# Kernel tuning notes

Hardware: AMD Instinct MI355X
Metric: run time of the kernel (lower is better)

## Reference

```python
import jax, jax.numpy as jnp
import numpy as np
import math

B, L, E, H = 512, 200, 64, 4
D = E // H
NEG = jnp.float32(-(2.0 ** 32) + 1.0)


def setup_inputs() -> dict:
    key = jax.random.key(0)
    ks = jax.random.split(key, 12)
    inp = jax.random.normal(ks[0], (B, L, E), dtype=jnp.float32)
    # realistic variable-length histories: mask[b, t] = t < len_b, len_b in [1, L]
    lens = jax.random.randint(ks[1], (B, 1), 1, L + 1)
    mask = jnp.arange(L)[None, :] < lens  # [B, L] bool
    s = 1.0 / math.sqrt(E)
    pos_enc = jax.random.normal(ks[2], (1, L, E), dtype=jnp.float32)
    Wk = jax.random.uniform(ks[3], (E, E), jnp.float32, -s, s)
    bk = jnp.zeros((E,), jnp.float32)
    Wv = jax.random.uniform(ks[4], (E, E), jnp.float32, -s, s)
    bv = jnp.zeros((E,), jnp.float32)
    Wq = jax.random.uniform(ks[5], (E, E), jnp.float32, -s, s)
    bq = jnp.zeros((E,), jnp.float32)
    Wf = jax.random.uniform(ks[6], (E, E), jnp.float32, -s, s)
    bf = jnp.zeros((E,), jnp.float32)
    return {"input": inp, "mask": mask, "pos_enc": pos_enc,
            "Wk": Wk, "bk": bk, "Wv": Wv, "bv": bv,
            "Wq": Wq, "bq": bq, "Wf": Wf, "bf": bf}


def reference(input, mask, pos_enc, Wk, bk, Wv, bv, Wq, bq, Wf, bf):
    x = input + pos_enc  # [B, L, E]
    # project and split heads: [B, H, L, D]
    def split(t):
        return t.reshape(B, L, H, D).transpose(0, 2, 1, 3)
    k = split(x @ Wk.T + bk)
    v = split(x @ Wv.T + bv)
    q = split(x @ Wq.T + bq) / math.sqrt(D)
    scores = jnp.einsum('bhqd,bhkd->bhqk', q, k)  # [B, H, L, L]
    # key_mask in torch code broadcasts over dim 3 (mask on the QUERY axis),
    # query_mask is its transpose (mask on the KEY axis). Combined: both must be valid.
    both = mask[:, None, :, None] & mask[:, None, None, :]  # [B, 1, L, L]
    scores = jnp.where(both, scores, NEG)
    attn = jax.nn.softmax(scores, axis=-1)
    # dropout is identity at inference; omitted deterministically
    out = jnp.einsum('bhqk,bhkd->bhqd', attn, v)
    out = out.transpose(0, 2, 1, 3).reshape(B, L, E)
    out = out @ Wf.T + bf
    fm = mask.astype(jnp.float32)[:, :, None]  # [B, L, 1]
    lens = jnp.sum(fm, axis=1)  # [B, 1]
    pooled = jnp.sum(out * fm, axis=1) / (lens + 1e-8)  # [B, E]
    return pooled
```

## Files before the change

kernel.cpp:

```cpp
#include <hip/hip_runtime.h>
#include <hip/hip_fp16.h>
#include <math.h>

#define Bn 512
#define Ln 200
#define En 64
#define Hn 4
#define Dn 16
#define KS3 18
#define VS3 200
#define QSC 0.36067376022224085f

typedef _Float16 __f16;
typedef __fp16 fp16x2 __attribute__((ext_vector_type(2)));
typedef __f16 f16x4 __attribute__((ext_vector_type(4)));
typedef __f16 f16x8 __attribute__((ext_vector_type(8)));
typedef float f32x4 __attribute__((ext_vector_type(4)));

#if __has_builtin(__builtin_amdgcn_exp2f)
__device__ __forceinline__ float fexp2(float x) { return __builtin_amdgcn_exp2f(x); }
#else
__device__ __forceinline__ float fexp2(float x) { return exp2f(x); }
#endif

__device__ __forceinline__ f16x8 pack8s(float4 a, float4 b, float4 pa, float4 pb) {
    f16x8 r;
    r[0] = (__f16)(a.x + pa.x); r[1] = (__f16)(a.y + pa.y);
    r[2] = (__f16)(a.z + pa.z); r[3] = (__f16)(a.w + pa.w);
    r[4] = (__f16)(b.x + pb.x); r[5] = (__f16)(b.y + pb.y);
    r[6] = (__f16)(b.z + pb.z); r[7] = (__f16)(b.w + pb.w);
    return r;
}
__device__ __forceinline__ f16x8 pack8(float4 a, float4 b) {
    f16x8 r;
    r[0] = (__f16)a.x; r[1] = (__f16)a.y; r[2] = (__f16)a.z; r[3] = (__f16)a.w;
    r[4] = (__f16)b.x; r[5] = (__f16)b.y; r[6] = (__f16)b.z; r[7] = (__f16)b.w;
    return r;
}

__device__ __forceinline__ f16x4 pack4rtz(float e0, float e1, float e2, float e3) {
    const fp16x2 lo = __builtin_amdgcn_cvt_pkrtz(e0, e1);
    const fp16x2 hi = __builtin_amdgcn_cvt_pkrtz(e2, e3);
    f16x4 r;
    r[0] = (__f16)lo[0]; r[1] = (__f16)lo[1];
    r[2] = (__f16)hi[0]; r[3] = (__f16)hi[1];
    return r;
}

template<int NI>
__device__ __forceinline__ void attn_core(
    const __f16* __restrict__ Kh_, const __f16* __restrict__ Qh_, const __f16* __restrict__ Vt_,
    int qt0, int klo, int khi, int nt, int len, int quad, int ln16,
    f32x4 (&o2)[4], f32x4 (&lacc)[4])
{
    const f16x4 ones = {(__f16)1.f, (__f16)1.f, (__f16)1.f, (__f16)1.f};
    f16x4 qf[NI];
    #pragma unroll
    for (int i = 0; i < NI; ++i) {
        int qr = min((qt0 + i) * 16 + ln16, Ln - 1);
        qf[i] = *(const f16x4*)(Qh_ + qr * KS3 + quad * 4);
    }
    const bool needmask = (khi == nt);
    const int kfull = khi - (needmask ? 1 : 0);

    f16x4 kf = *(const f16x4*)(Kh_ + min(klo * 16 + ln16, Ln - 1) * KS3 + quad * 4);
    f16x4 vf = *(const f16x4*)(Vt_ + ln16 * VS3 + min(klo * 16 + quad * 4, Ln - 4));

    for (int kt = klo; kt < kfull; ++kt) {
        const int krn = min((kt + 1) * 16 + ln16, Ln - 1);
        const int vcn = min((kt + 1) * 16 + quad * 4, Ln - 4);
        const f16x4 kfn = *(const f16x4*)(Kh_ + krn * KS3 + quad * 4);
        const f16x4 vfn = *(const f16x4*)(Vt_ + ln16 * VS3 + vcn);
        f32x4 s[NI];
        #pragma unroll
        for (int i = 0; i < NI; ++i)
            s[i] = __builtin_amdgcn_mfma_f32_16x16x16f16(kf, qf[i], (f32x4){0,0,0,0}, 0, 0, 0);
        f16x4 pf[NI];
        #pragma unroll
        for (int i = 0; i < NI; ++i) {
            pf[i] = pack4rtz(fexp2(fminf(s[i][0], 14.5f)),
                             fexp2(fminf(s[i][1], 14.5f)),
                             fexp2(fminf(s[i][2], 14.5f)),
                             fexp2(fminf(s[i][3], 14.5f)));
        }
        #pragma unroll
        for (int i = 0; i < NI; ++i) {
            o2[i]   = __builtin_amdgcn_mfma_f32_16x16x16f16(vf,   pf[i], o2[i],   0, 0, 0);
            lacc[i] = __builtin_amdgcn_mfma_f32_16x16x16f16(ones, pf[i], lacc[i], 0, 0, 0);
        }
        kf = kfn; vf = vfn;
    }
    if (needmask) {
        const int kbase = (nt - 1) * 16 + quad * 4;
        f32x4 s[NI];
        #pragma unroll
        for (int i = 0; i < NI; ++i)
            s[i] = __builtin_amdgcn_mfma_f32_16x16x16f16(kf, qf[i], (f32x4){0,0,0,0}, 0, 0, 0);
        f16x4 pf[NI];
        #pragma unroll
        for (int i = 0; i < NI; ++i) {
            float e[4];
            #pragma unroll
            for (int j = 0; j < 4; ++j) {
                const bool kok = (kbase + j) < len;
                e[j] = kok ? fexp2(fminf(s[i][j], 14.5f)) : 0.f;
            }
            pf[i] = pack4rtz(e[0], e[1], e[2], e[3]);
        }
        #pragma unroll
        for (int i = 0; i < NI; ++i) {
            o2[i]   = __builtin_amdgcn_mfma_f32_16x16x16f16(vf,   pf[i], o2[i],   0, 0, 0);
            lacc[i] = __builtin_amdgcn_mfma_f32_16x16x16f16(ones, pf[i], lacc[i], 0, 0, 0);
        }
    }
}

__global__ __launch_bounds__(256, 4) void fused_kernel(
    const float* __restrict__ input, const int* __restrict__ mask,
    const float* __restrict__ pos_enc,
    const float* __restrict__ Wk, const float* __restrict__ bk,
    const float* __restrict__ Wv, const float* __restrict__ bv,
    const float* __restrict__ Wq, const float* __restrict__ bq,
    const float* __restrict__ Wf, const float* __restrict__ bf_,
    float* __restrict__ out)
{
    __shared__ __align__(16) __f16 Kh[Ln * KS3];
    __shared__ __align__(16) __f16 Qh[Ln * KS3];
    __shared__ __align__(16) __f16 Vt[16 * VS3];
    __shared__ float lred[4][4][16];
    __shared__ float red[4][16];
    __shared__ float ph[16];
    __shared__ int cnt_red[4];

    const int tid  = threadIdx.x;
    const int qh   = blockIdx.x & 1;
    const int bh   = blockIdx.x >> 1;
    const int b    = bh >> 2, h = bh & 3;
    const int wave = tid >> 6, lane = tid & 63;
    const int quad = lane >> 4, ln16 = lane & 15;

    const int mv = (tid < Ln) ? mask[b * Ln + tid] : 0;

    int c = (mv != 0) ? 1 : 0;
    #pragma unroll
    for (int off = 32; off; off >>= 1) c += __shfl_down(c, off, 64);
    if (lane == 0) cnt_red[wave] = c;
    __syncthreads();
    const int len = cnt_red[0] + cnt_red[1] + cnt_red[2] + cnt_red[3];
    const int nt = (len + 15) >> 4;
    const int nquad = (nt + 3) >> 2;
    const bool split = (nquad >= 3);

    if (qh == 1 && !split) return;

    f16x8 bfr[3][2];
    #pragma unroll
    for (int m = 0; m < 3; ++m) {
        const float* W = (m == 0) ? Wk : (m == 1) ? Wv : Wq;
        #pragma unroll
        for (int ks = 0; ks < 2; ++ks) {
            const float4* wp = (const float4*)(W + (size_t)(h * 16 + ln16) * 64) + (ks * 8 + quad * 2);
            bfr[m][ks] = pack8(wp[0], wp[1]);
        }
    }
    const int cg = h * 16 + ln16;
    const float bkv = bk[cg], bvv = bv[cg], bqv = bq[cg];

    const float4* in4 = (const float4*)(input + (size_t)b * Ln * En);
    const float4* pe4 = (const float4*)pos_enc;

    for (int rt = wave; rt < nt; rt += 4) {
        const int R = rt * 16 + ln16;
        const bool rok = (R < Ln);
        f16x8 af[2];
        #pragma unroll
        for (int ks = 0; ks < 2; ++ks) {
            float4 xa = {0,0,0,0}, xb = {0,0,0,0}, pa = {0,0,0,0}, pb = {0,0,0,0};
            if (rok) {
                const int o4 = R * 16 + ks * 8 + quad * 2;
                xa = in4[o4]; xb = in4[o4 + 1];
                pa = pe4[o4]; pb = pe4[o4 + 1];
            }
            af[ks] = pack8s(xa, xb, pa, pb);
        }
        f32x4 acc[3];
        #pragma unroll
        for (int m = 0; m < 3; ++m) acc[m] = (f32x4){0,0,0,0};
        #pragma unroll
        for (int ks = 0; ks < 2; ++ks)
            #pragma unroll
            for (int m = 0; m < 3; ++m)
                acc[m] = __builtin_amdgcn_mfma_f32_16x16x32_f16(af[ks], bfr[m][ks], acc[m], 0, 0, 0);

        #pragma unroll
        for (int j = 0; j < 4; ++j) {
            const int t = rt * 16 + quad * 4 + j;
            if (t < Ln) {
                Kh[t * KS3 + ln16] = (__f16)(acc[0][j] + bkv);
                Qh[t * KS3 + ln16] = (__f16)((acc[2][j] + bqv) * QSC);
            }
        }
        const int vc0 = rt * 16 + quad * 4;
        if (vc0 < Ln) {
            f16x4 vp;
            #pragma unroll
            for (int j = 0; j < 4; ++j) vp[j] = (__f16)(acc[1][j] + bvv);
            *(f16x4*)(Vt + ln16 * VS3 + vc0) = vp;
        }
    }
    __syncthreads();

    int g, kh, nkh;
    if (split)            { g = qh + 2 * (wave & 1); kh = wave >> 1; nkh = 2; }
    else if (nquad == 2)  { g = wave & 1;            kh = wave >> 1; nkh = 2; }
    else                  { g = 0;                   kh = wave;      nkh = 4; }
    const bool active = (g < nquad);
    const int nktp = (nt + nkh - 1) / nkh;
    const int klo = kh * nktp;
    const int khi = min(klo + nktp, nt);
    const int qt0 = 4 * g;

    f32x4 o2[4], lacc[4];
    #pragma unroll
    for (int i = 0; i < 4; ++i) { o2[i] = (f32x4){0,0,0,0}; lacc[i] = (f32x4){0,0,0,0}; }

    if (active && klo < khi) {
        const int ni = __builtin_amdgcn_readfirstlane(min(4, nt - qt0));
        switch (ni) {
            case 1:  attn_core<1>(Kh, Qh, Vt, qt0, klo, khi, nt, len, quad, ln16, o2, lacc); break;
            case 2:  attn_core<2>(Kh, Qh, Vt, qt0, klo, khi, nt, len, quad, ln16, o2, lacc); break;
            case 3:  attn_core<3>(Kh, Qh, Vt, qt0, klo, khi, nt, len, quad, ln16, o2, lacc); break;
            default: attn_core<4>(Kh, Qh, Vt, qt0, klo, khi, nt, len, quad, ln16, o2, lacc); break;
        }
    }

    float l[4];
    #pragma unroll
    for (int i = 0; i < 4; ++i) l[i] = lacc[i][0];

    if (nkh > 1) {
        if (lane < 16) {
            #pragma unroll
            for (int i = 0; i < 4; ++i) lred[wave][i][lane] = l[i];
        }
        __syncthreads();
        const int slot = wave & 1;
        #pragma unroll
        for (int i = 0; i < 4; ++i) {
            if (nkh == 2) l[i] = lred[slot][i][ln16] + lred[slot + 2][i][ln16];
            else          l[i] = lred[0][i][ln16] + lred[1][i][ln16]
                               + lred[2][i][ln16] + lred[3][i][ln16];
        }
    }

    f32x4 pool = {0.f, 0.f, 0.f, 0.f};
    if (active) {
        #pragma unroll
        for (int i = 0; i < 4; ++i) {
            const float rs = ((qt0 + i) * 16 + ln16 < len) ? 1.f / l[i] : 0.f;
            #pragma unroll
            for (int j = 0; j < 4; ++j) pool[j] = fmaf(o2[i][j], rs, pool[j]);
        }
    }

    #pragma unroll
    for (int j = 0; j < 4; ++j) {
        #pragma unroll
        for (int off = 1; off < 16; off <<= 1) pool[j] += __shfl_xor(pool[j], off, 64);
    }
    if (ln16 == 0) {
        #pragma unroll
        for (int j = 0; j < 4; ++j) red[wave][quad * 4 + j] = pool[j];
    }
    __syncthreads();
    if (tid < 16)
        ph[tid] = (red[0][tid] + red[1][tid] + red[2][tid] + red[3][tid]) / ((float)len + 1e-8f);
    __syncthreads();

    if (tid < 64) {
        const int e = tid;
        const float* wr = Wf + (size_t)e * 64 + h * 16;
        float a = (h == 0 && qh == 0) ? bf_[e] : 0.f;
        #pragma unroll
        for (int i = 0; i < 16; ++i) a = fmaf(wr[i], ph[i], a);
        atomicAdd(out + b * En + e, a);
    }
}

extern "C" void kernel_launch(void* const* d_in, const int* in_sizes, int n_in,
                              void* d_out, int out_size, void* d_ws, size_t ws_size,
                              hipStream_t stream) {
    const float* input   = (const float*)d_in[0];
    const int*   mask    = (const int*)  d_in[1];
    const float* pos_enc = (const float*)d_in[2];
    const float* Wk      = (const float*)d_in[3];
    const float* bk      = (const float*)d_in[4];
    const float* Wv      = (const float*)d_in[5];
    const float* bv      = (const float*)d_in[6];
    const float* Wq      = (const float*)d_in[7];
    const float* bq      = (const float*)d_in[8];
    const float* Wf      = (const float*)d_in[9];
    const float* bf      = (const float*)d_in[10];

    float* out = (float*)d_out;
    hipMemsetAsync(out, 0, (size_t)Bn * En * sizeof(float), stream);

    fused_kernel<<<Bn * Hn * 2, 256, 0, stream>>>(input, mask, pos_enc,
                                                  Wk, bk, Wv, bv, Wq, bq, Wf, bf, out);
}
```

Before: 144.5 us.

## Use persistent producer/consumer crews with double-buffered QKV projection and attention

Replaces the one-block-per-(batch,head,half) launch with a persistent grid of 768 blocks of 512 threads. One 256-thread crew computes the QKV projection for the next item into a double-buffered LDS slot while the other crew runs attention and pooling on the current item. Each wave now owns a query group and covers all key tiles, which removes the cross-wave softmax-denominator reduction and the query-half split. The aim is to overlap global loads and projection with attention and to cut launch and per-block overhead. In exchange, LDS use doubles, the static item split can leave load imbalance across blocks, and each wave issues its own atomics.

Result: no change. 144.1 us (-0.3%).

```diff
diff --git a/kernel.cpp b/kernel.cpp
--- a/kernel.cpp
+++ b/kernel.cpp
@@ -6,7 +6,8 @@
 #define Ln 200
 #define En 64
 #define Hn 4
-#define Dn 16
+#define NITEMS (Bn * Hn)
+#define GRID 768
 #define KS3 18
 #define VS3 200
 #define QSC 0.36067376022224085f
@@ -115,7 +116,7 @@
     }
 }
 
-__global__ __launch_bounds__(256, 4) void fused_kernel(
+__global__ __launch_bounds__(512, 6) void fused_kernel(
     const float* __restrict__ input, const int* __restrict__ mask,
     const float* __restrict__ pos_enc,
     const float* __restrict__ Wk, const float* __restrict__ bk,
@@ -124,166 +125,159 @@
     const float* __restrict__ Wf, const float* __restrict__ bf_,
     float* __restrict__ out)
 {
-    __shared__ __align__(16) __f16 Kh[Ln * KS3];
-    __shared__ __align__(16) __f16 Qh[Ln * KS3];
-    __shared__ __align__(16) __f16 Vt[16 * VS3];
-    __shared__ float lred[4][4][16];
-    __shared__ float red[4][16];
-    __shared__ float ph[16];
-    __shared__ int cnt_red[4];
+    __shared__ __align__(16) __f16 KhB[2][Ln * KS3];
+    __shared__ __align__(16) __f16 QhB[2][Ln * KS3];
+    __shared__ __align__(16) __f16 VtB[2][16 * VS3];
+    __shared__ float swr[4][16];
+    __shared__ int meta[2];
 
     const int tid  = threadIdx.x;
-    const int qh   = blockIdx.x & 1;
-    const int bh   = blockIdx.x >> 1;
-    const int b    = bh >> 2, h = bh & 3;
-    const int wave = tid >> 6, lane = tid & 63;
+    const int crew = tid >> 8;
+    const int wv   = (tid >> 6) & 3;
+    const int lane = tid & 63;
     const int quad = lane >> 4, ln16 = lane & 15;
 
-    const int mv = (tid < Ln) ? mask[b * Ln + tid] : 0;
-
-    int c = (mv != 0) ? 1 : 0;
-    #pragma unroll
-    for (int off = 32; off; off >>= 1) c += __shfl_down(c, off, 64);
-    if (lane == 0) cnt_red[wave] = c;
-    __syncthreads();
-    const int len = cnt_red[0] + cnt_red[1] + cnt_red[2] + cnt_red[3];
-    const int nt = (len + 15) >> 4;
-    const int nquad = (nt + 3) >> 2;
-    const bool split = (nquad >= 3);
-
-    if (qh == 1 && !split) return;
-
-    f16x8 bfr[3][2];
-    #pragma unroll
-    for (int m = 0; m < 3; ++m) {
-        const float* W = (m == 0) ? Wk : (m == 1) ? Wv : Wq;
-        #pragma unroll
-        for (int ks = 0; ks < 2; ++ks) {
-            const float4* wp = (const float4*)(W + (size_t)(h * 16 + ln16) * 64) + (ks * 8 + quad * 2);
-            bfr[m][ks] = pack8(wp[0], wp[1]);
-        }
-    }
-    const int cg = h * 16 + ln16;
-    const float bkv = bk[cg], bvv = bv[cg], bqv = bq[cg];
-
-    const float4* in4 = (const float4*)(input + (size_t)b * Ln * En);
+    const int lin = (blockIdx.x & 7) * (GRID / 8) + (blockIdx.x >> 3);
+    const int m   = (lin < NITEMS - 2 * GRID) ? 3 : 2;
+
     const float4* pe4 = (const float4*)pos_enc;
 
-    for (int rt = wave; rt < nt; rt += 4) {
-        const int R = rt * 16 + ln16;
-        const bool rok = (R < Ln);
-        f16x8 af[2];
-        #pragma unroll
-        for (int ks = 0; ks < 2; ++ks) {
-            float4 xa = {0,0,0,0}, xb = {0,0,0,0}, pa = {0,0,0,0}, pb = {0,0,0,0};
-            if (rok) {
-                const int o4 = R * 16 + ks * 8 + quad * 2;
-                xa = in4[o4]; xb = in4[o4 + 1];
-                pa = pe4[o4]; pb = pe4[o4 + 1];
+    for (int j = -1; j < m; ++j) {
+        if (crew == 0) {
+            const int r = j + 1;
+            if (r < m) {
+                const int item = lin + r * GRID;
+                const int b = item >> 2, h = item & 3;
+                __f16* Kh = KhB[r & 1];
+                __f16* Qh = QhB[r & 1];
+                __f16* Vt = VtB[r & 1];
+                const float4* in4 = (const float4*)(input + (size_t)b * Ln * En);
+
+                const int* mb = mask + b * Ln;
+                int c = (mb[lane] != 0) + (mb[64 + lane] != 0) + (mb[128 + lane] != 0)
+                      + ((lane < Ln - 192) ? (mb[192 + lane] != 0) : 0);
+                #pragma unroll
+                for (int off = 32; off; off >>= 1) c += __shfl_down(c, off, 64);
+                const int len = __shfl(c, 0, 64);
+                const int nt = (len + 15) >> 4;
+                if (tid == 0) meta[r & 1] = len;
+
+                f16x8 bfr[3][2];
+                #pragma unroll
+                for (int mm = 0; mm < 3; ++mm) {
+                    const float* W = (mm == 0) ? Wk : (mm == 1) ? Wv : Wq;
+                    #pragma unroll
+                    for (int ks = 0; ks < 2; ++ks) {
+                        const float4* wp = (const float4*)(W + (size_t)(h * 16 + ln16) * 64) + (ks * 8 + quad * 2);
+                        bfr[mm][ks] = pack8(wp[0], wp[1]);
+                    }
+                }
+                const int cg = h * 16 + ln16;
+                const float bkv = bk[cg], bvv = bv[cg], bqv = bq[cg];
+
+                for (int rt = wv; rt < nt; rt += 4) {
+                    const int R = rt * 16 + ln16;
+                    const bool rok = (R < Ln);
+                    const int o4 = R * 16 + quad * 2;
+                    float4 xa = {0,0,0,0}, xb = {0,0,0,0}, xc = {0,0,0,0}, xd = {0,0,0,0};
+                    float4 pa = {0,0,0,0}, pb = {0,0,0,0}, pc = {0,0,0,0}, pd = {0,0,0,0};
+                    if (rok) {
+                        xa = in4[o4];     xb = in4[o4 + 1];
+                        xc = in4[o4 + 8]; xd = in4[o4 + 9];
+                        pa = pe4[o4];     pb = pe4[o4 + 1];
+                        pc = pe4[o4 + 8]; pd = pe4[o4 + 9];
+                    }
+                    const f16x8 af0 = pack8s(xa, xb, pa, pb);
+                    const f16x8 af1 = pack8s(xc, xd, pc, pd);
+
+                    f32x4 acc[3];
+                    #pragma unroll
+                    for (int mm = 0; mm < 3; ++mm) acc[mm] = (f32x4){0,0,0,0};
+                    #pragma unroll
+                    for (int mm = 0; mm < 3; ++mm)
+                        acc[mm] = __builtin_amdgcn_mfma_f32_16x16x32_f16(af0, bfr[mm][0], acc[mm], 0, 0, 0);
+                    #pragma unroll
+                    for (int mm = 0; mm < 3; ++mm)
+                        acc[mm] = __builtin_amdgcn_mfma_f32_16x16x32_f16(af1, bfr[mm][1], acc[mm], 0, 0, 0);
+
+                    #pragma unroll
+                    for (int jj = 0; jj < 4; ++jj) {
+                        const int t = rt * 16 + quad * 4 + jj;
+                        if (t < Ln) {
+                            Kh[t * KS3 + ln16] = (__f16)(acc[0][jj] + bkv);
+                            Qh[t * KS3 + ln16] = (__f16)((acc[2][jj] + bqv) * QSC);
+                        }
+                    }
+                    const int vc0 = rt * 16 + quad * 4;
+                    if (vc0 < Ln) {
+                        f16x4 vp;
+                        #pragma unroll
+                        for (int jj = 0; jj < 4; ++jj) vp[jj] = (__f16)(acc[1][jj] + bvv);
+                        *(f16x4*)(Vt + ln16 * VS3 + vc0) = vp;
+                    }
+                }
             }
-            af[ks] = pack8s(xa, xb, pa, pb);
-        }
-        f32x4 acc[3];
-        #pragma unroll
-        for (int m = 0; m < 3; ++m) acc[m] = (f32x4){0,0,0,0};
-        #pragma unroll
-        for (int ks = 0; ks < 2; ++ks)
-            #pragma unroll
-            for (int m = 0; m < 3; ++m)
-                acc[m] = __builtin_amdgcn_mfma_f32_16x16x32_f16(af[ks], bfr[m][ks], acc[m], 0, 0, 0);
-
-        #pragma unroll
-        for (int j = 0; j < 4; ++j) {
-            const int t = rt * 16 + quad * 4 + j;
-            if (t < Ln) {
-                Kh[t * KS3 + ln16] = (__f16)(acc[0][j] + bkv);
-                Qh[t * KS3 + ln16] = (__f16)((acc[2][j] + bqv) * QSC);
+        } else {
+            if (j >= 0) {
+                const int item = lin + j * GRID;
+                const int b = item >> 2, h = item & 3;
+                const __f16* Kh = KhB[j & 1];
+                const __f16* Qh = QhB[j & 1];
+                const __f16* Vt = VtB[j & 1];
+                const int len = meta[j & 1];
+                const int nt = (len + 15) >> 4;
+                const int nquad = (nt + 3) >> 2;
+                const int g = wv;
+                const int qt0 = 4 * g;
+                const bool active = (g < nquad);
+
+                f32x4 o2[4], lacc[4];
+                #pragma unroll
+                for (int i = 0; i < 4; ++i) { o2[i] = (f32x4){0,0,0,0}; lacc[i] = (f32x4){0,0,0,0}; }
+
+                if (active) {
+                    const int ni = __builtin_amdgcn_readfirstlane(min(4, nt - qt0));
+                    switch (ni) {
+                        case 1:  attn_core<1>(Kh, Qh, Vt, qt0, 0, nt, nt, len, quad, ln16, o2, lacc); break;
+                        case 2:  attn_core<2>(Kh, Qh, Vt, qt0, 0, nt, nt, len, quad, ln16, o2, lacc); break;
+                        case 3:  attn_core<3>(Kh, Qh, Vt, qt0, 0, nt, nt, len, quad, ln16, o2, lacc); break;
+                        default: attn_core<4>(Kh, Qh, Vt, qt0, 0, nt, nt, len, quad, ln16, o2, lacc); break;
+                    }
+                }
+
+                f32x4 pool = {0.f, 0.f, 0.f, 0.f};
+                if (active) {
+                    #pragma unroll
+                    for (int i = 0; i < 4; ++i) {
+                        const float rs = ((qt0 + i) * 16 + ln16 < len) ? 1.f / lacc[i][0] : 0.f;
+                        #pragma unroll
+                        for (int jj = 0; jj < 4; ++jj) pool[jj] = fmaf(o2[i][jj], rs, pool[jj]);
+                    }
+                }
+                #pragma unroll
+                for (int jj = 0; jj < 4; ++jj) {
+                    #pragma unroll
+                    for (int off = 1; off < 16; off <<= 1) pool[jj] += __shfl_xor(pool[jj], off, 64);
+                }
+                if (ln16 == 0) {
+                    #pragma unroll
+                    for (int jj = 0; jj < 4; ++jj) swr[wv][quad * 4 + jj] = pool[jj];
+                }
+                float phv[16];
+                #pragma unroll
+                for (int i = 0; i < 16; ++i) phv[i] = swr[wv][i];
+
+                const float invlen = 1.f / ((float)len + 1e-8f);
+                const float* wr = Wf + (size_t)lane * En + h * 16;
+                float a = 0.f;
+                #pragma unroll
+                for (int i = 0; i < 16; ++i) a = fmaf(wr[i], phv[i], a);
+                a *= invlen;
+                if (h == 0 && wv == 0) a += bf_[lane];
+                atomicAdd(out + b * En + lane, a);
             }
         }
-        const int vc0 = rt * 16 + quad * 4;
-        if (vc0 < Ln) {
-            f16x4 vp;
-            #pragma unroll
-            for (int j = 0; j < 4; ++j) vp[j] = (__f16)(acc[1][j] + bvv);
-            *(f16x4*)(Vt + ln16 * VS3 + vc0) = vp;
-        }
-    }
-    __syncthreads();
-
-    int g, kh, nkh;
-    if (split)            { g = qh + 2 * (wave & 1); kh = wave >> 1; nkh = 2; }
-    else if (nquad == 2)  { g = wave & 1;            kh = wave >> 1; nkh = 2; }
-    else                  { g = 0;                   kh = wave;      nkh = 4; }
-    const bool active = (g < nquad);
-    const int nktp = (nt + nkh - 1) / nkh;
-    const int klo = kh * nktp;
-    const int khi = min(klo + nktp, nt);
-    const int qt0 = 4 * g;
-
-    f32x4 o2[4], lacc[4];
-    #pragma unroll
-    for (int i = 0; i < 4; ++i) { o2[i] = (f32x4){0,0,0,0}; lacc[i] = (f32x4){0,0,0,0}; }
-
-    if (active && klo < khi) {
-        const int ni = __builtin_amdgcn_readfirstlane(min(4, nt - qt0));
-        switch (ni) {
-            case 1:  attn_core<1>(Kh, Qh, Vt, qt0, klo, khi, nt, len, quad, ln16, o2, lacc); break;
-            case 2:  attn_core<2>(Kh, Qh, Vt, qt0, klo, khi, nt, len, quad, ln16, o2, lacc); break;
-            case 3:  attn_core<3>(Kh, Qh, Vt, qt0, klo, khi, nt, len, quad, ln16, o2, lacc); break;
-            default: attn_core<4>(Kh, Qh, Vt, qt0, klo, khi, nt, len, quad, ln16, o2, lacc); break;
-        }
-    }
-
-    float l[4];
-    #pragma unroll
-    for (int i = 0; i < 4; ++i) l[i] = lacc[i][0];
-
-    if (nkh > 1) {
-        if (lane < 16) {
-            #pragma unroll
-            for (int i = 0; i < 4; ++i) lred[wave][i][lane] = l[i];
-        }
         __syncthreads();
-        const int slot = wave & 1;
-        #pragma unroll
-        for (int i = 0; i < 4; ++i) {
-            if (nkh == 2) l[i] = lred[slot][i][ln16] + lred[slot + 2][i][ln16];
-            else          l[i] = lred[0][i][ln16] + lred[1][i][ln16]
-                               + lred[2][i][ln16] + lred[3][i][ln16];
-        }
-    }
-
-    f32x4 pool = {0.f, 0.f, 0.f, 0.f};
-    if (active) {
-        #pragma unroll
-        for (int i = 0; i < 4; ++i) {
-            const float rs = ((qt0 + i) * 16 + ln16 < len) ? 1.f / l[i] : 0.f;
-            #pragma unroll
-            for (int j = 0; j < 4; ++j) pool[j] = fmaf(o2[i][j], rs, pool[j]);
-        }
-    }
-
-    #pragma unroll
-    for (int j = 0; j < 4; ++j) {
-        #pragma unroll
-        for (int off = 1; off < 16; off <<= 1) pool[j] += __shfl_xor(pool[j], off, 64);
-    }
-    if (ln16 == 0) {
-        #pragma unroll
-        for (int j = 0; j < 4; ++j) red[wave][quad * 4 + j] = pool[j];
-    }
-    __syncthreads();
-    if (tid < 16)
-        ph[tid] = (red[0][tid] + red[1][tid] + red[2][tid] + red[3][tid]) / ((float)len + 1e-8f);
-    __syncthreads();
-
-    if (tid < 64) {
-        const int e = tid;
-        const float* wr = Wf + (size_t)e * 64 + h * 16;
-        float a = (h == 0 && qh == 0) ? bf_[e] : 0.f;
-        #pragma unroll
-        for (int i = 0; i < 16; ++i) a = fmaf(wr[i], ph[i], a);
-        atomicAdd(out + b * En + e, a);
     }
 }
 
@@ -305,6 +299,6 @@
     float* out = (float*)d_out;
     hipMemsetAsync(out, 0, (size_t)Bn * En * sizeof(float), stream);
 
-    fused_kernel<<<Bn * Hn * 2, 256, 0, stream>>>(input, mask, pos_enc,
-                                                  Wk, bk, Wv, bv, Wq, bq, Wf, bf, out);
-}
+    fused_kernel<<<GRID, 512, 0, stream>>>(input, mask, pos_enc,
+                                           Wk, bk, Wv, bv, Wq, bq, Wf, bf, out);
+}
```
